# Optimization experiments

Measured on AMD Instinct MI355X. Metric: run time of the kernel, lower is better.

The kernel has to match this reference:

```python
import jax, jax.numpy as jnp
import numpy as np

N_SRC = 50000
N_DST = 50000
E = 800000
D = 128
OUT = 128


def setup_inputs() -> dict:
    key = jax.random.key(0)
    k1, k2, k3, k4, k5, k6 = jax.random.split(key, 6)
    lim = 1.0 / np.sqrt(D)
    return {
        "x_src": jax.random.normal(k1, (N_SRC, D), dtype=jnp.float32),
        "x_dst": jax.random.normal(k2, (N_DST, D), dtype=jnp.float32),
        "edge_src": jax.random.randint(k3, (E,), 0, N_SRC, dtype=jnp.int64),
        "edge_dst": jax.random.randint(k4, (E,), 0, N_DST, dtype=jnp.int64),
        "num_dst": N_DST,
        # learned params (torch nn.Linear: y = x @ W.T + b), stored here as [in, out]
        "W_neigh": jax.random.uniform(k5, (D, OUT), jnp.float32, -lim, lim),
        "b_neigh": jnp.zeros((OUT,), jnp.float32),
        "W_self": jax.random.uniform(k6, (D, OUT), jnp.float32, -lim, lim),
        "b_self": jnp.zeros((OUT,), jnp.float32),
    }


def reference(x_src, x_dst, edge_src, edge_dst, num_dst, W_neigh, b_neigh, W_self, b_self):
    # gather source features per edge: [E, D]
    neigh_feats = x_src[edge_src]
    # scatter-mean onto destination nodes
    summed = jax.ops.segment_sum(neigh_feats, edge_dst, num_segments=num_dst)  # [num_dst, D]
    count = jax.ops.segment_sum(jnp.ones((edge_dst.shape[0], 1), x_src.dtype), edge_dst,
                                num_segments=num_dst)
    agg = summed / jnp.clip(count, 1.0)
    # dual linear + add
    return agg @ W_neigh + b_neigh + x_dst @ W_self + b_self
```

## Files before the change

### kernel.cpp

```cpp
#include <hip/hip_runtime.h>

#define D 128
#define TM 64
#define CBITS 7
#define CSIZE 128
#define MAXNB 512
#define CAPB 2560

typedef __attribute__((ext_vector_type(8))) short bf16x8;
typedef __attribute__((ext_vector_type(4))) float f32x4;


__device__ __forceinline__ unsigned short f32_to_bf16(float x) {
    unsigned u = __float_as_uint(x);
    u += 0x7FFFu + ((u >> 16) & 1u);
    return (unsigned short)(u >> 16);
}
__device__ __forceinline__ float bf16_to_f32(unsigned short h) {
    return __uint_as_float(((unsigned)h) << 16);
}

__global__ __launch_bounds__(256) void prep_kernel(
    const float* __restrict__ Wn, const float* __restrict__ Ws,
    unsigned short* __restrict__ Wtn, unsigned short* __restrict__ Wts,
    int* __restrict__ gcursor, int NB) {
    const int stride = gridDim.x * 256;
    for (int i = blockIdx.x * 256 + threadIdx.x; i < D * D; i += stride) {
        int n = i >> 7, k = i & (D - 1);
        Wtn[i] = f32_to_bf16(Wn[k * D + n]);
        Wts[i] = f32_to_bf16(Ws[k * D + n]);
    }
    for (int i = blockIdx.x * 256 + threadIdx.x; i < NB; i += stride)
        gcursor[i] = 0;
}

__global__ __launch_bounds__(256) void fused_part_gemm_kernel(
    const int* __restrict__ edge_src, const int* __restrict__ edge_dst,
    int* __restrict__ gcursor, int* __restrict__ packed, int E, int NB,
    const float* __restrict__ x_src, const float* __restrict__ x_dst,
    const unsigned short* __restrict__ Wtn, const unsigned short* __restrict__ Wts,
    const float* __restrict__ bn, const float* __restrict__ bs,
    unsigned short* __restrict__ y16, float* __restrict__ out,
    int M_SRC, int N, int nblk, int blkA, int pstride) {
    __shared__ __align__(16) char smem[TM * 136 * 2 + D * 136 * 2];
    const int t = threadIdx.x;
    const int idx = (int)blockIdx.x;

    const bool isPart = (idx % pstride == 0) && (idx / pstride < nblk);

    if (isPart) {
        const int pid = idx / pstride;
        int* lh    = (int*)smem;
        int* lbase = lh + MAXNB;
        for (int i = t; i < NB; i += 256) lh[i] = 0;
        __syncthreads();
        const int base = pid * 2048;
        int es[8], ed[8];
        #pragma unroll
        for (int i = 0; i < 8; ++i) {
            int e = base + t + i * 256;
            if (e < E) { es[i] = edge_src[e]; ed[i] = edge_dst[e]; }
            else ed[i] = -1;
        }
        #pragma unroll
        for (int i = 0; i < 8; ++i)
            if (ed[i] >= 0) atomicAdd(&lh[ed[i] >> CBITS], 1);
        __syncthreads();
        for (int i = t; i < NB; i += 256) {
            int v = lh[i];
            lbase[i] = v ? atomicAdd(&gcursor[i], v) : 0;
        }
        __syncthreads();
        for (int i = t; i < NB; i += 256) lh[i] = 0;
        __syncthreads();
        #pragma unroll
        for (int i = 0; i < 8; ++i) {
            if (ed[i] >= 0) {
                int bk = ed[i] >> CBITS;
                int pos = lbase[bk] + atomicAdd(&lh[bk], 1);
                if (pos < CAPB)
                    packed[(size_t)bk * CAPB + pos] =
                        (es[i] << CBITS) | (ed[i] & (CSIZE - 1));
            }
        }
        return;
    }

    typedef unsigned short ushort136[136];
    ushort136* LA = (ushort136*)smem;
    ushort136* LW = (ushort136*)(smem + TM * 136 * 2);

    const int npb  = min((idx + pstride - 1) / pstride, nblk);
    const int gb   = idx - npb;
    const bool isA  = gb < blkA;
    const int  row0 = (isA ? gb : gb - blkA) * TM;
    const int  M    = isA ? M_SRC : N;
    const float* Ap = isA ? x_src : x_dst;
    const unsigned short* Wp = isA ? Wtn : Wts;

    {
        const float4* Av = (const float4*)Ap;
        #pragma unroll
        for (int i = 0; i < 8; ++i) {
            int vi = t + i * 256;
            int r = vi >> 5, c4 = vi & 31;
            int sr = min(row0 + r, M - 1);
            float4 v = Av[(size_t)sr * 32 + c4];
            ushort4 p;
            p.x = f32_to_bf16(v.x); p.y = f32_to_bf16(v.y);
            p.z = f32_to_bf16(v.z); p.w = f32_to_bf16(v.w);
            *(ushort4*)&LA[r][c4 * 4] = p;
        }
        const int4* Wv = (const int4*)Wp;
        #pragma unroll
        for (int i = 0; i < 8; ++i) {
            int vi = t + i * 256;
            int r = vi >> 4, c8 = vi & 15;
            *(int4*)&LW[r][c8 * 8] = Wv[vi];
        }
    }
    __syncthreads();

    const int lane = t & 63;
    const int wv   = t >> 6;
    const int wr   = wv & 1;
    const int wc   = wv >> 1;
    const int lr   = lane & 15;
    const int g    = lane >> 4;

    f32x4 acc[2][4];
    #pragma unroll
    for (int i = 0; i < 2; ++i)
        #pragma unroll
        for (int j = 0; j < 4; ++j) acc[i][j] = (f32x4){0.f, 0.f, 0.f, 0.f};

    #pragma unroll
    for (int kt = 0; kt < 4; ++kt) {
        bf16x8 b0 = *(const bf16x8*)&LW[wc * 64 + 0 * 16 + lr][kt * 32 + g * 8];
        bf16x8 b1 = *(const bf16x8*)&LW[wc * 64 + 1 * 16 + lr][kt * 32 + g * 8];
        bf16x8 b2 = *(const bf16x8*)&LW[wc * 64 + 2 * 16 + lr][kt * 32 + g * 8];
        bf16x8 b3 = *(const bf16x8*)&LW[wc * 64 + 3 * 16 + lr][kt * 32 + g * 8];
        bf16x8 a0 = *(const bf16x8*)&LA[wr * 32 + lr][kt * 32 + g * 8];
        bf16x8 a1 = *(const bf16x8*)&LA[wr * 32 + 16 + lr][kt * 32 + g * 8];
        acc[0][0] = __builtin_amdgcn_mfma_f32_16x16x32_bf16(a0, b0, acc[0][0], 0, 0, 0);
        acc[0][1] = __builtin_amdgcn_mfma_f32_16x16x32_bf16(a0, b1, acc[0][1], 0, 0, 0);
        acc[0][2] = __builtin_amdgcn_mfma_f32_16x16x32_bf16(a0, b2, acc[0][2], 0, 0, 0);
        acc[0][3] = __builtin_amdgcn_mfma_f32_16x16x32_bf16(a0, b3, acc[0][3], 0, 0, 0);
        acc[1][0] = __builtin_amdgcn_mfma_f32_16x16x32_bf16(a1, b0, acc[1][0], 0, 0, 0);
        acc[1][1] = __builtin_amdgcn_mfma_f32_16x16x32_bf16(a1, b1, acc[1][1], 0, 0, 0);
        acc[1][2] = __builtin_amdgcn_mfma_f32_16x16x32_bf16(a1, b2, acc[1][2], 0, 0, 0);
        acc[1][3] = __builtin_amdgcn_mfma_f32_16x16x32_bf16(a1, b3, acc[1][3], 0, 0, 0);
    }

    if (isA) {
        #pragma unroll
        for (int i = 0; i < 2; ++i) {
            #pragma unroll
            for (int j = 0; j < 4; ++j) {
                int col = wc * 64 + j * 16 + lr;
                #pragma unroll
                for (int r = 0; r < 4; ++r) {
                    int row = row0 + wr * 32 + i * 16 + g * 4 + r;
                    if (row < M)
                        y16[(size_t)row * D + col] = f32_to_bf16(acc[i][j][r]);
                }
            }
        }
    } else {
        #pragma unroll
        for (int i = 0; i < 2; ++i) {
            #pragma unroll
            for (int j = 0; j < 4; ++j) {
                int col = wc * 64 + j * 16 + lr;
                float bias = bn[col] + bs[col];
                #pragma unroll
                for (int r = 0; r < 4; ++r) {
                    int row = row0 + wr * 32 + i * 16 + g * 4 + r;
                    if (row < M)
                        out[(size_t)row * D + col] = acc[i][j][r] + bias;
                }
            }
        }
    }
}

__global__ __launch_bounds__(512) void fine_kernel(
    const int* __restrict__ packed, const int* __restrict__ gcursor,
    int* __restrict__ off_beg, int* __restrict__ off_end,
    int* __restrict__ eidx, int N) {
    __shared__ int dcount[8][CSIZE];
    __shared__ int wbase[8][CSIZE];
    __shared__ int sbuf[CSIZE];
    const int b  = blockIdx.x;
    const int d0 = b << CBITS;
    const int beg = b * CAPB;
    const int cnt = min(gcursor[b], CAPB);
    const int t = threadIdx.x;
    const int wv = t >> 6;

    if (t < CSIZE) {
        #pragma unroll
        for (int w = 0; w < 8; ++w) dcount[w][t] = 0;
    }
    __syncthreads();
    for (int i = t; i < cnt; i += 512)
        atomicAdd(&dcount[wv][packed[beg + i] & (CSIZE - 1)], 1);
    __syncthreads();
    int tot = 0;
    if (t < CSIZE) {
        #pragma unroll
        for (int w = 0; w < 8; ++w) tot += dcount[w][t];
        sbuf[t] = tot;
    }
    __syncthreads();
    for (int ofs = 1; ofs < CSIZE; ofs <<= 1) {
        int u = (t < CSIZE && t >= ofs) ? sbuf[t - ofs] : 0;
        __syncthreads();
        if (t < CSIZE) sbuf[t] += u;
        __syncthreads();
    }
    if (t < CSIZE) {
        int excl = sbuf[t] - tot;
        int d = d0 + t;
        if (d < N) {
            off_beg[d] = beg + excl;
            off_end[d] = beg + excl + tot;
        }
        int run = excl;
        #pragma unroll
        for (int w = 0; w < 8; ++w) {
            wbase[w][t] = run;
            run += dcount[w][t];
        }
    }
    __syncthreads();
    for (int i = t; i < cnt; i += 512) {
        int p = packed[beg + i];
        int pos = beg + atomicAdd(&wbase[wv][p & (CSIZE - 1)], 1);
        eidx[pos] = p >> CBITS;
    }
}

__global__ __launch_bounds__(256) void gather_out_kernel(
    const unsigned short* __restrict__ y16,
    const int* __restrict__ off_beg,
    const int* __restrict__ off_end,
    const int* __restrict__ eidx,
    float* __restrict__ out, int N) {
    const int wave = (int)(((long long)blockIdx.x * blockDim.x + threadIdx.x) >> 6);
    const int lane = threadIdx.x & 63;
    if (wave >= N) return;
    const int h = lane >> 4;
    const int c = lane & 15;
    const int beg = off_beg[wave];
    const int end = off_end[wave];

    float acc[8];
    #pragma unroll
    for (int j = 0; j < 8; ++j) acc[j] = 0.f;

    int i = beg + h;
    for (; i + 4 < end; i += 8) {
        int s0 = eidx[i];
        int s1 = eidx[i + 4];
        const int4 v0 = *reinterpret_cast<const int4*>(y16 + (size_t)s0 * D + c * 8);
        const int4 v1 = *reinterpret_cast<const int4*>(y16 + (size_t)s1 * D + c * 8);
        const unsigned short* h0 = (const unsigned short*)&v0;
        const unsigned short* h1 = (const unsigned short*)&v1;
        #pragma unroll
        for (int j = 0; j < 8; ++j)
            acc[j] += bf16_to_f32(h0[j]) + bf16_to_f32(h1[j]);
    }
    if (i < end) {
        int s = eidx[i];
        const int4 v = *reinterpret_cast<const int4*>(y16 + (size_t)s * D + c * 8);
        const unsigned short* hs = (const unsigned short*)&v;
        #pragma unroll
        for (int j = 0; j < 8; ++j) acc[j] += bf16_to_f32(hs[j]);
    }

    #pragma unroll
    for (int j = 0; j < 8; ++j) {
        acc[j] += __shfl_down(acc[j], 32);
        acc[j] += __shfl_down(acc[j], 16);
    }

    if (h == 0) {
        const float inv = 1.0f / fmaxf((float)(end - beg), 1.0f);
        float4* o = reinterpret_cast<float4*>(out + (size_t)wave * D) + c * 2;
        float4 c0 = o[0], c1 = o[1];
        c0.x = fmaf(acc[0], inv, c0.x);
        c0.y = fmaf(acc[1], inv, c0.y);
        c0.z = fmaf(acc[2], inv, c0.z);
        c0.w = fmaf(acc[3], inv, c0.w);
        c1.x = fmaf(acc[4], inv, c1.x);
        c1.y = fmaf(acc[5], inv, c1.y);
        c1.z = fmaf(acc[6], inv, c1.z);
        c1.w = fmaf(acc[7], inv, c1.w);
        o[0] = c0;
        o[1] = c1;
    }
}

extern "C" void kernel_launch(void* const* d_in, const int* in_sizes, int n_in,
                              void* d_out, int out_size, void* d_ws, size_t ws_size,
                              hipStream_t stream) {
    const float* x_src    = (const float*)d_in[0];
    const float* x_dst    = (const float*)d_in[1];
    const int*   edge_src = (const int*)d_in[2];
    const int*   edge_dst = (const int*)d_in[3];
    const float* Wn = (const float*)d_in[5];
    const float* bn = (const float*)d_in[6];
    const float* Ws = (const float*)d_in[7];
    const float* bs = (const float*)d_in[8];

    const int E     = in_sizes[2];
    const int N     = in_sizes[1] / D;
    const int M_SRC = in_sizes[0] / D;

    const int NB   = (N + CSIZE - 1) >> CBITS;
    const int nblk = (E + 2047) / 2048;

    unsigned short* y16 = (unsigned short*)d_ws;
    unsigned short* Wtn = y16 + (size_t)M_SRC * D;
    unsigned short* Wts = Wtn + D * D;
    int* packed  = (int*)(Wts + D * D);
    int* eidx    = packed + (size_t)NB * CAPB;
    int* off_beg = eidx + (size_t)NB * CAPB;
    int* off_end = off_beg + N;
    int* gcursor = off_end + N;

    const int T = 256;
    prep_kernel<<<32, T, 0, stream>>>(Wn, Ws, Wtn, Wts, gcursor, NB);

    const int blkA = (M_SRC + TM - 1) / TM;
    const int blkB = (N + TM - 1) / TM;
    const int total = nblk + blkA + blkB;
    const int pstride = total / nblk > 1 ? total / nblk : 1;
    fused_part_gemm_kernel<<<total, T, 0, stream>>>(
        edge_src, edge_dst, gcursor, packed, E, NB,
        x_src, x_dst, Wtn, Wts, bn, bs, y16, (float*)d_out,
        M_SRC, N, nblk, blkA, pstride);

    fine_kernel<<<NB, 512, 0, stream>>>(packed, gcursor, off_beg, off_end, eidx, N);

    gather_out_kernel<<<(N + 3) / 4, T, 0, stream>>>(
        y16, off_beg, off_end, eidx, (float*)d_out, N);
}
```

Baseline: 73.84 us.

## Aggregate raw bf16 source features first, then run one fused dual GEMM

```diff
diff --git a/kernel.cpp b/kernel.cpp
--- a/kernel.cpp
+++ b/kernel.cpp
@@ -6,6 +6,7 @@
 #define CSIZE 128
 #define MAXNB 512
 #define CAPB 2560
+#define CASTBLK 256
 
 typedef __attribute__((ext_vector_type(8))) short bf16x8;
 typedef __attribute__((ext_vector_type(4))) float f32x4;
@@ -18,6 +19,18 @@
 }
 __device__ __forceinline__ float bf16_to_f32(unsigned short h) {
     return __uint_as_float(((unsigned)h) << 16);
+}
+__device__ __forceinline__ int4 pack8_bf16(const float* v) {
+    ushort2 a = {f32_to_bf16(v[0]), f32_to_bf16(v[1])};
+    ushort2 b = {f32_to_bf16(v[2]), f32_to_bf16(v[3])};
+    ushort2 c = {f32_to_bf16(v[4]), f32_to_bf16(v[5])};
+    ushort2 d = {f32_to_bf16(v[6]), f32_to_bf16(v[7])};
+    int4 r;
+    r.x = (int)(a.x | ((unsigned)a.y << 16));
+    r.y = (int)(b.x | ((unsigned)b.y << 16));
+    r.z = (int)(c.x | ((unsigned)c.y << 16));
+    r.w = (int)(d.x | ((unsigned)d.y << 16));
+    return r;
 }
 
 __global__ __launch_bounds__(256) void prep_kernel(
@@ -34,27 +47,20 @@
         gcursor[i] = 0;
 }
 
-__global__ __launch_bounds__(256) void fused_part_gemm_kernel(
+__global__ __launch_bounds__(256) void part_cast_kernel(
     const int* __restrict__ edge_src, const int* __restrict__ edge_dst,
     int* __restrict__ gcursor, int* __restrict__ packed, int E, int NB,
-    const float* __restrict__ x_src, const float* __restrict__ x_dst,
-    const unsigned short* __restrict__ Wtn, const unsigned short* __restrict__ Wts,
-    const float* __restrict__ bn, const float* __restrict__ bs,
-    unsigned short* __restrict__ y16, float* __restrict__ out,
-    int M_SRC, int N, int nblk, int blkA, int pstride) {
-    __shared__ __align__(16) char smem[TM * 136 * 2 + D * 136 * 2];
+    const float* __restrict__ x_src, unsigned short* __restrict__ xsrc16,
+    int M_SRC, int nblk) {
+    __shared__ int lh[MAXNB];
+    __shared__ int lbase[MAXNB];
     const int t = threadIdx.x;
     const int idx = (int)blockIdx.x;
 
-    const bool isPart = (idx % pstride == 0) && (idx / pstride < nblk);
-
-    if (isPart) {
-        const int pid = idx / pstride;
-        int* lh    = (int*)smem;
-        int* lbase = lh + MAXNB;
+    if (idx < nblk) {
         for (int i = t; i < NB; i += 256) lh[i] = 0;
         __syncthreads();
-        const int base = pid * 2048;
+        const int base = idx * 2048;
         int es[8], ed[8];
         #pragma unroll
         for (int i = 0; i < 8; ++i) {
@@ -86,101 +92,14 @@
         return;
     }
 
-    typedef unsigned short ushort136[136];
-    ushort136* LA = (ushort136*)smem;
-    ushort136* LW = (ushort136*)(smem + TM * 136 * 2);
-
-    const int npb  = min((idx + pstride - 1) / pstride, nblk);
-    const int gb   = idx - npb;
-    const bool isA  = gb < blkA;
-    const int  row0 = (isA ? gb : gb - blkA) * TM;
-    const int  M    = isA ? M_SRC : N;
-    const float* Ap = isA ? x_src : x_dst;
-    const unsigned short* Wp = isA ? Wtn : Wts;
-
-    {
-        const float4* Av = (const float4*)Ap;
-        #pragma unroll
-        for (int i = 0; i < 8; ++i) {
-            int vi = t + i * 256;
-            int r = vi >> 5, c4 = vi & 31;
-            int sr = min(row0 + r, M - 1);
-            float4 v = Av[(size_t)sr * 32 + c4];
-            ushort4 p;
-            p.x = f32_to_bf16(v.x); p.y = f32_to_bf16(v.y);
-            p.z = f32_to_bf16(v.z); p.w = f32_to_bf16(v.w);
-            *(ushort4*)&LA[r][c4 * 4] = p;
-        }
-        const int4* Wv = (const int4*)Wp;
-        #pragma unroll
-        for (int i = 0; i < 8; ++i) {
-            int vi = t + i * 256;
-            int r = vi >> 4, c8 = vi & 15;
-            *(int4*)&LW[r][c8 * 8] = Wv[vi];
-        }
-    }
-    __syncthreads();
-
-    const int lane = t & 63;
-    const int wv   = t >> 6;
-    const int wr   = wv & 1;
-    const int wc   = wv >> 1;
-    const int lr   = lane & 15;
-    const int g    = lane >> 4;
-
-    f32x4 acc[2][4];
-    #pragma unroll
-    for (int i = 0; i < 2; ++i)
-        #pragma unroll
-        for (int j = 0; j < 4; ++j) acc[i][j] = (f32x4){0.f, 0.f, 0.f, 0.f};
-
-    #pragma unroll
-    for (int kt = 0; kt < 4; ++kt) {
-        bf16x8 b0 = *(const bf16x8*)&LW[wc * 64 + 0 * 16 + lr][kt * 32 + g * 8];
-        bf16x8 b1 = *(const bf16x8*)&LW[wc * 64 + 1 * 16 + lr][kt * 32 + g * 8];
-        bf16x8 b2 = *(const bf16x8*)&LW[wc * 64 + 2 * 16 + lr][kt * 32 + g * 8];
-        bf16x8 b3 = *(const bf16x8*)&LW[wc * 64 + 3 * 16 + lr][kt * 32 + g * 8];
-        bf16x8 a0 = *(const bf16x8*)&LA[wr * 32 + lr][kt * 32 + g * 8];
-        bf16x8 a1 = *(const bf16x8*)&LA[wr * 32 + 16 + lr][kt * 32 + g * 8];
-        acc[0][0] = __builtin_amdgcn_mfma_f32_16x16x32_bf16(a0, b0, acc[0][0], 0, 0, 0);
-        acc[0][1] = __builtin_amdgcn_mfma_f32_16x16x32_bf16(a0, b1, acc[0][1], 0, 0, 0);
-        acc[0][2] = __builtin_amdgcn_mfma_f32_16x16x32_bf16(a0, b2, acc[0][2], 0, 0, 0);
-        acc[0][3] = __builtin_amdgcn_mfma_f32_16x16x32_bf16(a0, b3, acc[0][3], 0, 0, 0);
-        acc[1][0] = __builtin_amdgcn_mfma_f32_16x16x32_bf16(a1, b0, acc[1][0], 0, 0, 0);
-        acc[1][1] = __builtin_amdgcn_mfma_f32_16x16x32_bf16(a1, b1, acc[1][1], 0, 0, 0);
-        acc[1][2] = __builtin_amdgcn_mfma_f32_16x16x32_bf16(a1, b2, acc[1][2], 0, 0, 0);
-        acc[1][3] = __builtin_amdgcn_mfma_f32_16x16x32_bf16(a1, b3, acc[1][3], 0, 0, 0);
-    }
-
-    if (isA) {
-        #pragma unroll
-        for (int i = 0; i < 2; ++i) {
-            #pragma unroll
-            for (int j = 0; j < 4; ++j) {
-                int col = wc * 64 + j * 16 + lr;
-                #pragma unroll
-                for (int r = 0; r < 4; ++r) {
-                    int row = row0 + wr * 32 + i * 16 + g * 4 + r;
-                    if (row < M)
-                        y16[(size_t)row * D + col] = f32_to_bf16(acc[i][j][r]);
-                }
-            }
-        }
-    } else {
-        #pragma unroll
-        for (int i = 0; i < 2; ++i) {
-            #pragma unroll
-            for (int j = 0; j < 4; ++j) {
-                int col = wc * 64 + j * 16 + lr;
-                float bias = bn[col] + bs[col];
-                #pragma unroll
-                for (int r = 0; r < 4; ++r) {
-                    int row = row0 + wr * 32 + i * 16 + g * 4 + r;
-                    if (row < M)
-                        out[(size_t)row * D + col] = acc[i][j][r] + bias;
-                }
-            }
-        }
+    const int cid = idx - nblk;
+    const size_t total8 = (size_t)M_SRC * D / 8;
+    for (size_t i = (size_t)cid * 256 + t; i < total8;
+         i += (size_t)CASTBLK * 256) {
+        const float4* src = ((const float4*)x_src) + i * 2;
+        float4 p0 = src[0], p1 = src[1];
+        float v[8] = {p0.x, p0.y, p0.z, p0.w, p1.x, p1.y, p1.z, p1.w};
+        ((int4*)xsrc16)[i] = pack8_bf16(v);
     }
 }
 
@@ -241,12 +160,12 @@
     }
 }
 
-__global__ __launch_bounds__(256) void gather_out_kernel(
-    const unsigned short* __restrict__ y16,
+__global__ __launch_bounds__(256) void gather_agg_kernel(
+    const unsigned short* __restrict__ xsrc16,
     const int* __restrict__ off_beg,
     const int* __restrict__ off_end,
     const int* __restrict__ eidx,
-    float* __restrict__ out, int N) {
+    unsigned short* __restrict__ agg16, int N) {
     const int wave = (int)(((long long)blockIdx.x * blockDim.x + threadIdx.x) >> 6);
     const int lane = threadIdx.x & 63;
     if (wave >= N) return;
@@ -263,8 +182,8 @@
     for (; i + 4 < end; i += 8) {
         int s0 = eidx[i];
         int s1 = eidx[i + 4];
-        const int4 v0 = *reinterpret_cast<const int4*>(y16 + (size_t)s0 * D + c * 8);
-        const int4 v1 = *reinterpret_cast<const int4*>(y16 + (size_t)s1 * D + c * 8);
+        const int4 v0 = *reinterpret_cast<const int4*>(xsrc16 + (size_t)s0 * D + c * 8);
+        const int4 v1 = *reinterpret_cast<const int4*>(xsrc16 + (size_t)s1 * D + c * 8);
         const unsigned short* h0 = (const unsigned short*)&v0;
         const unsigned short* h1 = (const unsigned short*)&v1;
         #pragma unroll
@@ -273,7 +192,7 @@
     }
     if (i < end) {
         int s = eidx[i];
-        const int4 v = *reinterpret_cast<const int4*>(y16 + (size_t)s * D + c * 8);
+        const int4 v = *reinterpret_cast<const int4*>(xsrc16 + (size_t)s * D + c * 8);
         const unsigned short* hs = (const unsigned short*)&v;
         #pragma unroll
         for (int j = 0; j < 8; ++j) acc[j] += bf16_to_f32(hs[j]);
@@ -287,18 +206,111 @@
 
     if (h == 0) {
         const float inv = 1.0f / fmaxf((float)(end - beg), 1.0f);
-        float4* o = reinterpret_cast<float4*>(out + (size_t)wave * D) + c * 2;
-        float4 c0 = o[0], c1 = o[1];
-        c0.x = fmaf(acc[0], inv, c0.x);
-        c0.y = fmaf(acc[1], inv, c0.y);
-        c0.z = fmaf(acc[2], inv, c0.z);
-        c0.w = fmaf(acc[3], inv, c0.w);
-        c1.x = fmaf(acc[4], inv, c1.x);
-        c1.y = fmaf(acc[5], inv, c1.y);
-        c1.z = fmaf(acc[6], inv, c1.z);
-        c1.w = fmaf(acc[7], inv, c1.w);
-        o[0] = c0;
-        o[1] = c1;
+        float v[8];
+        #pragma unroll
+        for (int j = 0; j < 8; ++j) v[j] = acc[j] * inv;
+        *(int4*)(agg16 + (size_t)wave * D + c * 8) = pack8_bf16(v);
+    }
+}
+
+__global__ __launch_bounds__(256) void gemm_final_kernel(
+    const unsigned short* __restrict__ agg16,
+    const float* __restrict__ x_dst,
+    const unsigned short* __restrict__ Wtn, const unsigned short* __restrict__ Wts,
+    const float* __restrict__ bn, const float* __restrict__ bs,
+    float* __restrict__ out, int N) {
+    __shared__ unsigned short LAa[TM][136];
+    __shared__ unsigned short LAx[TM][136];
+    const int t = threadIdx.x;
+    const int row0 = blockIdx.x * TM;
+
+    #pragma unroll
+    for (int i = 0; i < 4; ++i) {
+        int vi = t + i * 256;
+        int r = vi >> 4, c8 = vi & 15;
+        int sr = min(row0 + r, N - 1);
+        *(int4*)&LAa[r][c8 * 8] =
+            *(const int4*)(agg16 + (size_t)sr * D + c8 * 8);
+    }
+    {
+        const float4* Av = (const float4*)x_dst;
+        #pragma unroll
+        for (int i = 0; i < 8; ++i) {
+            int vi = t + i * 256;
+            int r = vi >> 5, c4 = vi & 31;
+            int sr = min(row0 + r, N - 1);
+            float4 v = Av[(size_t)sr * 32 + c4];
+            ushort4 p;
+            p.x = f32_to_bf16(v.x); p.y = f32_to_bf16(v.y);
+            p.z = f32_to_bf16(v.z); p.w = f32_to_bf16(v.w);
+            *(ushort4*)&LAx[r][c4 * 4] = p;
+        }
+    }
+    __syncthreads();
+
+    const int lane = t & 63;
+    const int wv   = t >> 6;
+    const int wr   = wv & 1;
+    const int wc   = wv >> 1;
+    const int lr   = lane & 15;
+    const int g    = lane >> 4;
+
+    f32x4 acc[2][4];
+    #pragma unroll
+    for (int i = 0; i < 2; ++i)
+        #pragma unroll
+        for (int j = 0; j < 4; ++j) acc[i][j] = (f32x4){0.f, 0.f, 0.f, 0.f};
+
+    #pragma unroll
+    for (int kt = 0; kt < 4; ++kt) {
+        const int kk = kt * 32 + g * 8;
+        bf16x8 b0 = *(const bf16x8*)&Wtn[(size_t)(wc * 64 + 0 * 16 + lr) * D + kk];
+        bf16x8 b1 = *(const bf16x8*)&Wtn[(size_t)(wc * 64 + 1 * 16 + lr) * D + kk];
+        bf16x8 b2 = *(const bf16x8*)&Wtn[(size_t)(wc * 64 + 2 * 16 + lr) * D + kk];
+        bf16x8 b3 = *(const bf16x8*)&Wtn[(size_t)(wc * 64 + 3 * 16 + lr) * D + kk];
+        bf16x8 a0 = *(const bf16x8*)&LAa[wr * 32 + lr][kk];
+        bf16x8 a1 = *(const bf16x8*)&LAa[wr * 32 + 16 + lr][kk];
+        acc[0][0] = __builtin_amdgcn_mfma_f32_16x16x32_bf16(a0, b0, acc[0][0], 0, 0, 0);
+        acc[0][1] = __builtin_amdgcn_mfma_f32_16x16x32_bf16(a0, b1, acc[0][1], 0, 0, 0);
+        acc[0][2] = __builtin_amdgcn_mfma_f32_16x16x32_bf16(a0, b2, acc[0][2], 0, 0, 0);
+        acc[0][3] = __builtin_amdgcn_mfma_f32_16x16x32_bf16(a0, b3, acc[0][3], 0, 0, 0);
+        acc[1][0] = __builtin_amdgcn_mfma_f32_16x16x32_bf16(a1, b0, acc[1][0], 0, 0, 0);
+        acc[1][1] = __builtin_amdgcn_mfma_f32_16x16x32_bf16(a1, b1, acc[1][1], 0, 0, 0);
+        acc[1][2] = __builtin_amdgcn_mfma_f32_16x16x32_bf16(a1, b2, acc[1][2], 0, 0, 0);
+        acc[1][3] = __builtin_amdgcn_mfma_f32_16x16x32_bf16(a1, b3, acc[1][3], 0, 0, 0);
+    }
+    #pragma unroll
+    for (int kt = 0; kt < 4; ++kt) {
+        const int kk = kt * 32 + g * 8;
+        bf16x8 b0 = *(const bf16x8*)&Wts[(size_t)(wc * 64 + 0 * 16 + lr) * D + kk];
+        bf16x8 b1 = *(const bf16x8*)&Wts[(size_t)(wc * 64 + 1 * 16 + lr) * D + kk];
+        bf16x8 b2 = *(const bf16x8*)&Wts[(size_t)(wc * 64 + 2 * 16 + lr) * D + kk];
+        bf16x8 b3 = *(const bf16x8*)&Wts[(size_t)(wc * 64 + 3 * 16 + lr) * D + kk];
+        bf16x8 a0 = *(const bf16x8*)&LAx[wr * 32 + lr][kk];
+        bf16x8 a1 = *(const bf16x8*)&LAx[wr * 32 + 16 + lr][kk];
+        acc[0][0] = __builtin_amdgcn_mfma_f32_16x16x32_bf16(a0, b0, acc[0][0], 0, 0, 0);
+        acc[0][1] = __builtin_amdgcn_mfma_f32_16x16x32_bf16(a0, b1, acc[0][1], 0, 0, 0);
+        acc[0][2] = __builtin_amdgcn_mfma_f32_16x16x32_bf16(a0, b2, acc[0][2], 0, 0, 0);
+        acc[0][3] = __builtin_amdgcn_mfma_f32_16x16x32_bf16(a0, b3, acc[0][3], 0, 0, 0);
+        acc[1][0] = __builtin_amdgcn_mfma_f32_16x16x32_bf16(a1, b0, acc[1][0], 0, 0, 0);
+        acc[1][1] = __builtin_amdgcn_mfma_f32_16x16x32_bf16(a1, b1, acc[1][1], 0, 0, 0);
+        acc[1][2] = __builtin_amdgcn_mfma_f32_16x16x32_bf16(a1, b2, acc[1][2], 0, 0, 0);
+        acc[1][3] = __builtin_amdgcn_mfma_f32_16x16x32_bf16(a1, b3, acc[1][3], 0, 0, 0);
+    }
+
+    #pragma unroll
+    for (int i = 0; i < 2; ++i) {
+        #pragma unroll
+        for (int j = 0; j < 4; ++j) {
+            int col = wc * 64 + j * 16 + lr;
+            float bias = bn[col] + bs[col];
+            #pragma unroll
+            for (int r = 0; r < 4; ++r) {
+                int row = row0 + wr * 32 + i * 16 + g * 4 + r;
+                if (row < N)
+                    out[(size_t)row * D + col] = acc[i][j][r] + bias;
+            }
+        }
     }
 }
 
@@ -321,29 +333,32 @@
     const int NB   = (N + CSIZE - 1) >> CBITS;
     const int nblk = (E + 2047) / 2048;
 
-    unsigned short* y16 = (unsigned short*)d_ws;
-    unsigned short* Wtn = y16 + (size_t)M_SRC * D;
-    unsigned short* Wts = Wtn + D * D;
-    int* packed  = (int*)(Wts + D * D);
-    int* eidx    = packed + (size_t)NB * CAPB;
+    unsigned short* xsrc16 = (unsigned short*)d_ws;
+    char* regionB = (char*)(xsrc16 + (size_t)M_SRC * D);
+    int* packed          = (int*)regionB;
+    unsigned short* agg16 = (unsigned short*)regionB;
+    size_t bBytes = (size_t)NB * CAPB * 4;
+    size_t aBytes = (size_t)N * D * 2;
+    if (aBytes > bBytes) bBytes = aBytes;
+    int* eidx    = (int*)(regionB + bBytes);
     int* off_beg = eidx + (size_t)NB * CAPB;
     int* off_end = off_beg + N;
     int* gcursor = off_end + N;
+    unsigned short* Wtn = (unsigned short*)(gcursor + NB);
+    unsigned short* Wts = Wtn + D * D;
 
     const int T = 256;
     prep_kernel<<<32, T, 0, stream>>>(Wn, Ws, Wtn, Wts, gcursor, NB);
 
-    const int blkA = (M_SRC + TM - 1) / TM;
-    const int blkB = (N + TM - 1) / TM;
-    const int total = nblk + blkA + blkB;
-    const int pstride = total / nblk > 1 ? total / nblk : 1;
-    fused_part_gemm_kernel<<<total, T, 0, stream>>>(
+    part_cast_kernel<<<nblk + CASTBLK, T, 0, stream>>>(
         edge_src, edge_dst, gcursor, packed, E, NB,
-        x_src, x_dst, Wtn, Wts, bn, bs, y16, (float*)d_out,
-        M_SRC, N, nblk, blkA, pstride);
+        x_src, xsrc16, M_SRC, nblk);
 
     fine_kernel<<<NB, 512, 0, stream>>>(packed, gcursor, off_beg, off_end, eidx, N);
 
-    gather_out_kernel<<<(N + 3) / 4, T, 0, stream>>>(
-        y16, off_beg, off_end, eidx, (float*)d_out, N);
-}
+    gather_agg_kernel<<<(N + 3) / 4, T, 0, stream>>>(
+        xsrc16, off_beg, off_end, eidx, agg16, N);
+
+    gemm_final_kernel<<<(N + TM - 1) / TM, T, 0, stream>>>(
+        agg16, x_dst, Wtn, Wts, bn, bs, (float*)d_out, N);
+}
```

After: 91.62 us. +24.1%, slower.
